# Kernel optimization log

Measured on AMD Instinct MI355X. Metric: run time of the kernel, lower is better.

## Reference

```python
import jax, jax.numpy as jnp
import numpy as np
import math

# Static config (mirrors init_kwargs)
E, B, S, D, F, HMAX = 8, 4, 1024, 1024, 4096, 8
W = 768                      # active slimmable width (multiple giving integer head_dim)
H = max(1, W * HMAX // D)    # = 6 heads at width 768
HD = W // H                  # = 128
TOPK = 2
EPS = 1e-6


def setup_inputs() -> dict:
    key = jax.random.key(0)
    ks = jax.random.split(key, 14)
    sd = 1.0 / math.sqrt(D)
    sf = 1.0 / math.sqrt(F)
    return {
        "x":  jax.random.normal(ks[0], (B, S, D), jnp.float32),
        "wr": jax.random.normal(ks[1], (D, E), jnp.float32) * sd,
        "qw": jax.random.normal(ks[2], (E, D, D), jnp.float32) * sd,
        "qb": jax.random.normal(ks[3], (E, D), jnp.float32) * sd,
        "kw": jax.random.normal(ks[4], (E, D, D), jnp.float32) * sd,
        "kb": jax.random.normal(ks[5], (E, D), jnp.float32) * sd,
        "vw": jax.random.normal(ks[6], (E, D, D), jnp.float32) * sd,
        "vb": jax.random.normal(ks[7], (E, D), jnp.float32) * sd,
        "ow": jax.random.normal(ks[8], (E, D, D), jnp.float32) * sd,
        "ob": jax.random.normal(ks[9], (E, D), jnp.float32) * sd,
        "w1": jax.random.normal(ks[10], (E, F, D), jnp.float32) * sd,
        "b1": jax.random.normal(ks[11], (E, F), jnp.float32) * sd,
        "w2": jax.random.normal(ks[12], (E, D, F), jnp.float32) * sf,
        "b2": jax.random.normal(ks[13], (E, D), jnp.float32) * sf,
    }


def _slim_linear(x, w, b, in_w, out_w):
    # SlimmableLinear: dynamically slice max-size weight/bias to active widths
    return x @ w[:out_w, :in_w].T + b[:out_w]


def _rms_norm(x):
    # SlimmableExpert._layer_norm: RMS normalization (no mean-subtract, no affine)
    var = jnp.mean(jnp.square(x), axis=-1, keepdims=True)
    return x / jnp.sqrt(var + EPS)


def _expert_fwd(x_s, qw, qb, kw, kb, vw, vb, ow, ob, w1, b1, w2, b2):
    # x_s: [B, S, W]  (already sliced to active width)
    # --- slimmable self-attention at width W ---
    q = _slim_linear(x_s, qw, qb, W, W).reshape(B, S, H, HD).transpose(0, 2, 1, 3)
    k = _slim_linear(x_s, kw, kb, W, W).reshape(B, S, H, HD).transpose(0, 2, 1, 3)
    v = _slim_linear(x_s, vw, vb, W, W).reshape(B, S, H, HD).transpose(0, 2, 1, 3)
    scores = jnp.einsum('bhqd,bhkd->bhqk', q, k) / math.sqrt(HD)   # [B,H,S,S]
    attn = jax.nn.softmax(scores, axis=-1)
    ao = jnp.einsum('bhqk,bhkd->bhqd', attn, v)
    ao = ao.transpose(0, 2, 1, 3).reshape(B, S, W)
    ao = _slim_linear(ao, ow, ob, W, W)
    x1 = _rms_norm(x_s + ao)
    # --- slimmable FFN: W -> F (full) -> W, exact GELU (torch default) ---
    h = jax.nn.gelu(_slim_linear(x1, w1, b1, W, F), approximate=False)
    f = _slim_linear(h, w2, b2, F, W)
    return _rms_norm(x1 + f)   # [B,S,W]


def reference(x, wr, qw, qb, kw, kb, vw, vb, ow, ob, w1, b1, w2, b2):
    # Router: softmax over experts, top-k dispatch with renormalized gates
    logits = jnp.einsum('bsd,de->bse', x, wr)            # [B,S,E]
    probs = jax.nn.softmax(logits, axis=-1)
    topv, topi = jax.lax.top_k(probs, TOPK)              # [B,S,K]
    topv = topv / jnp.sum(topv, axis=-1, keepdims=True)
    bi = jnp.arange(B)[:, None, None]
    si = jnp.arange(S)[None, :, None]
    gate = jnp.zeros((B, S, E), x.dtype).at[bi, si, topi].set(topv)  # sparse gate

    # Slice tokens to active width (width embedding skipped: closest stored
    # width 736 != 768, per source shape-match check)
    x_s = x[..., :W]
    outs = []
    for e in range(E):   # small fixed expert count; bounds peak memory
        outs.append(_expert_fwd(x_s, qw[e], qb[e], kw[e], kb[e], vw[e], vb[e],
                                ow[e], ob[e], w1[e], b1[e], w2[e], b2[e]))
    eo = jnp.stack(outs, axis=0)                          # [E,B,S,W]
    out_w = jnp.einsum('bse,ebsw->bsw', gate, eo)         # gate-weighted combine
    # Zero-pad sliced width back to full model dim (per SlimmableExpert)
    out = jnp.concatenate(
        [out_w, jnp.zeros((B, S, D - W), x.dtype)], axis=-1)
    return out
```

## Files before the change

kernel.cpp:

```cpp
#include <hip/hip_runtime.h>
#include <cstdint>

#define NE 8
#define NB 4
#define NS 1024
#define ND 1024
#define NF 4096
#define NW 768
#define NH 6
#define NHD 128
#define NTOK 4096
#define NBH 24
#define RCAP 10496
#define VSTRIDE ((size_t)NTOK * NW)
#define EPS 1e-6f

typedef unsigned short ush;
typedef __attribute__((ext_vector_type(8))) short short8;
typedef __attribute__((ext_vector_type(4))) float f32x4;
typedef __attribute__((ext_vector_type(4))) unsigned short u16x4;

typedef const __attribute__((address_space(1))) void gvoid_t;
typedef __attribute__((address_space(3))) void lvoid_t;

__device__ __forceinline__ void gload16(const void* g, void* l) {
  __builtin_amdgcn_global_load_lds((gvoid_t*)g, (lvoid_t*)l, 16, 0, 0);
}

__device__ __forceinline__ ush f2b(float f) {
  union { float f; uint32_t u; } x; x.f = f;
  uint32_t r = x.u + 0x7fffu + ((x.u >> 16) & 1u);
  return (ush)(r >> 16);
}
__device__ __forceinline__ float b2f(ush u) {
  union { uint32_t u; float f; } x; x.u = (uint32_t)u << 16;
  return x.f;
}
__device__ __forceinline__ int prefix_sum(const int* __restrict__ c, int n) {
  int s = 0;
#pragma unroll 1
  for (int i = 0; i < n; ++i) s += c[i];
  return s;
}


__global__ __launch_bounds__(256, 4)
void router_kernel(const float* __restrict__ x, const float* __restrict__ wr,
                   float* __restrict__ gate, int* __restrict__ inv) {
  int lane = threadIdx.x & 63, wave = threadIdx.x >> 6;
  int t = blockIdx.x * 4 + wave;
  float acc[NE] = {};
  for (int i = 0; i < 16; ++i) {
    int d = lane + i * 64;
    float xv = x[(size_t)t * ND + d];
    const float* wp = wr + (size_t)d * NE;
    float4 w0 = *(const float4*)wp, w1 = *(const float4*)(wp + 4);
    acc[0] += xv * w0.x; acc[1] += xv * w0.y; acc[2] += xv * w0.z; acc[3] += xv * w0.w;
    acc[4] += xv * w1.x; acc[5] += xv * w1.y; acc[6] += xv * w1.z; acc[7] += xv * w1.w;
  }
#pragma unroll
  for (int e = 0; e < NE; ++e)
    for (int m = 1; m < 64; m <<= 1) acc[e] += __shfl_xor(acc[e], m);
  int i1 = 0; float v1 = acc[0];
#pragma unroll
  for (int e = 1; e < NE; ++e) if (acc[e] > v1) { v1 = acc[e]; i1 = e; }
  int i2 = -1; float v2 = -3.0e38f;
#pragma unroll
  for (int e = 0; e < NE; ++e) if (e != i1 && acc[e] > v2) { v2 = acc[e]; i2 = e; }
  float p2 = __expf(v2 - v1);
  float g1 = 1.0f / (1.0f + p2), g2 = p2 / (1.0f + p2);
  if (lane < NE)
    gate[(size_t)t * NE + lane] = (lane == i1) ? g1 : ((lane == i2) ? g2 : 0.0f);
  if (lane < 2) inv[t * 2 + lane] = -1;
}

__global__ __launch_bounds__(1024, 1)
void build_index(const float* __restrict__ gate, int* __restrict__ cnt64s,
                 int* __restrict__ idx_all, int* __restrict__ inv) {
  int e = blockIdx.x >> 2, b = blockIdx.x & 3;
  int s = threadIdx.x, t = b * 1024 + s;
  bool on = gate[(size_t)t * NE + e] > 0.0f;
  idx_all[(e * 4 + b) * 1024 + s] = (b * 1024) | (int)0x80000000;
  __shared__ int wsum[16], wbase[16];
  unsigned long long mask = __ballot(on);
  int lane = s & 63, wv = s >> 6;
  if (lane == 0) wsum[wv] = __popcll(mask);
  __syncthreads();
  if (s == 0) {
    int acc = 0;
    for (int i = 0; i < 16; ++i) { wbase[i] = acc; acc += wsum[i]; }
    cnt64s[e * 4 + b] = (acc + 63) & ~63;
  }
  __syncthreads();
  if (on) {
    int pos = wbase[wv] + __popcll(mask & ((1ull << lane) - 1ull));
    idx_all[(e * 4 + b) * 1024 + pos] = t;
    int k = 0;
#pragma unroll
    for (int j = 0; j < NE; ++j) k += (j < e && gate[(size_t)t * NE + j] > 0.0f);
    inv[t * 2 + k] = (e << 12) | pos;
  }
}

__global__ __launch_bounds__(256, 4)
void cast_all(const float* __restrict__ x,
              const float* __restrict__ qw, const float* __restrict__ kw,
              const float* __restrict__ vw, const float* __restrict__ ow,
              const float* __restrict__ w1, const float* __restrict__ w2,
              ush* __restrict__ xs,
              ush* __restrict__ dq, ush* __restrict__ dk, ush* __restrict__ dv,
              ush* __restrict__ dwo, ush* __restrict__ d1, ush* __restrict__ d2) {
  int y = blockIdx.y;
  if (y == 8) {
    const int n4 = NTOK * NW / 4;
    for (int u = blockIdx.x * 256 + threadIdx.x; u < n4; u += gridDim.x * 256) {
      int r = u / (NW / 4), c = u - r * (NW / 4);
      float4 v = *(const float4*)(x + (size_t)r * ND + c * 4);
      u16x4 o; o.x = f2b(v.x); o.y = f2b(v.y); o.z = f2b(v.z); o.w = f2b(v.w);
      *(u16x4*)(xs + (size_t)u * 4) = o;
    }
    return;
  }
  const int e = y;
  const int Q4 = 147456;
  const int W14 = 786432;
  const int total = 4 * Q4 + 2 * W14;
  const float* qe = qw + (size_t)e * ND * ND;
  const float* ke = kw + (size_t)e * ND * ND;
  const float* ve = vw + (size_t)e * ND * ND;
  const float* oe = ow + (size_t)e * ND * ND;
  const float* w1e = w1 + (size_t)e * NF * ND;
  const float* w2e = w2 + (size_t)e * ND * NF;
  ush* dqe = dq + (size_t)e * NW * NW;
  ush* dke = dk + (size_t)e * NW * NW;
  ush* dve = dv + (size_t)e * NW * NW;
  ush* doe = dwo + (size_t)e * NW * NW;
  ush* d1e = d1 + (size_t)e * NF * NW;
  ush* d2e = d2 + (size_t)e * NW * NF;
  for (int u = blockIdx.x * 256 + threadIdx.x; u < total; u += gridDim.x * 256) {
    const float* src; ush* dst; int ldsrc, cols4, rel;
    if (u < 4 * Q4) {
      int which = u / Q4; rel = u - which * Q4;
      src = (which == 0) ? qe : (which == 1) ? ke : (which == 2) ? ve : oe;
      dst = (which == 0) ? dqe : (which == 1) ? dke : (which == 2) ? dve : doe;
      ldsrc = 1024; cols4 = 192;
    } else if (u < 4 * Q4 + W14) {
      rel = u - 4 * Q4; src = w1e; dst = d1e; ldsrc = 1024; cols4 = 192;
    } else {
      rel = u - 4 * Q4 - W14; src = w2e; dst = d2e; ldsrc = 4096; cols4 = 1024;
    }
    int r = rel / cols4, c = rel - r * cols4;
    float4 v = *(const float4*)(src + (size_t)r * ldsrc + (size_t)c * 4);
    u16x4 o; o.x = f2b(v.x); o.y = f2b(v.y); o.z = f2b(v.z); o.w = f2b(v.w);
    *(u16x4*)(dst + (size_t)rel * 4) = o;
  }
}

#define BM 128
#define BN 128

__device__ __forceinline__ float gelu_fast(float v) {
  float u = v * fmaf(0.0356774081f, v * v, 0.7978845608f);
  float p = __expf(2.0f * fabsf(u));
  float th = fmaf(-2.0f, __builtin_amdgcn_rcpf(p + 1.0f), 1.0f);
  th = copysignf(th, u);
  return 0.5f * v * (1.0f + th);
}

__device__ __forceinline__ void stage_geom(int tid, int c, int& row, int& kb) {
  int v = (c & 1) * 32 + (tid >> 3);
  int b67 = ((tid >> 2) & 1) ^ ((v >> 2) & 1);
  row = v + 64 * b67;
  kb = ((tid ^ v) & 3) << 4;
}

__global__ __launch_bounds__(256, 3)
void qkv_gemm(const ush* __restrict__ A,
              const ush* __restrict__ wqb, const ush* __restrict__ wkb,
              const ush* __restrict__ wvb,
              const float* __restrict__ qbias, const float* __restrict__ kbias,
              const float* __restrict__ vbias,
              ush* __restrict__ qg, ush* __restrict__ kg, ush* __restrict__ vtg,
              const int* __restrict__ cnt64s, const int* __restrict__ idx_all) {
  const int bid = blockIdx.x;
  const int e = bid & 7, wi = bid >> 3;
  const int bn = wi % 6, bm = (wi / 6) % 32, w = wi / 192;
  int sb = 0, cnt = 0;
  if (w == 0) {
    int sec = e * 4 + (bm >> 3);
    cnt = cnt64s[sec];
    if (((bm & 7) * 128) >= cnt) return;
    sb = prefix_sum(cnt64s, sec);
  }
  const ush* Bw = ((w == 0) ? wqb : (w == 1) ? wkb : wvb) + (size_t)e * NW * NW;
  const float* bias = ((w == 0) ? qbias : (w == 1) ? kbias : vbias) + (size_t)e * ND;

  __shared__ __align__(16) char LDS[3 * 16384];

  const int tid = threadIdx.x, lane = tid & 63, wave = tid >> 6;
  const int lr = lane & 15, lg = lane >> 4;
  const int wr = wave >> 1, wc = wave & 1;

  size_t srcOff[4];
#pragma unroll
  for (int c = 0; c < 4; ++c) {
    int row, kb; stage_geom(tid, c, row, kb);
    int gRow;
    if (c < 2) {
      if (w == 0) {
        int lrow = (bm & 7) * 128 + row;
        gRow = idx_all[(e * 4 + (bm >> 3)) * 1024 + lrow] & 0x7fffffff;
      } else {
        gRow = bm * BM + row;
      }
    } else {
      gRow = bn * BN + row;
    }
    srcOff[c] = (size_t)gRow * (NW * 2) + kb;
  }

  int offA[4], offB[4];
#pragma unroll
  for (int i = 0; i < 4; ++i) {
    offA[i] = (i * 16 + lr) * 128 + (((wr << 6) | (lg << 4)) ^ ((lr & 7) << 4));
    offB[i] = (i * 16 + lr) * 128 + (((wc << 6) | (lg << 4)) ^ ((lr & 7) << 4)) + 8192;
  }

  auto stg = [&](int slot, int kt) {
    size_t kOff = (size_t)kt * 64;
    char* dst = LDS + slot * 16384;
#pragma unroll
    for (int c = 0; c < 4; ++c) {
      const char* src = (c < 2) ? (const char*)A + srcOff[c] + kOff
                                : (const char*)Bw + srcOff[c] + kOff;
      gload16(src, dst + c * 4096 + tid * 16);
    }
  };

  f32x4 acc[4][4] = {};
  const int nkt = NW / 32;
  stg(0, 0); stg(1, 1);
  asm volatile("s_waitcnt vmcnt(4)" ::: "memory");
  asm volatile("s_barrier" ::: "memory");
  int slot = 0;
  for (int kt = 0; kt < nkt; ++kt) {
    int s2 = slot + 2; if (s2 >= 3) s2 -= 3;
    bool more = (kt + 2 < nkt);
    if (more) stg(s2, kt + 2);
    const char* base = LDS + slot * 16384;
    short8 af[4], bfr[4];
#pragma unroll
    for (int i = 0; i < 4; ++i) {
      af[i] = *(const short8*)(base + offA[i]);
      bfr[i] = *(const short8*)(base + offB[i]);
    }
#pragma unroll
    for (int i = 0; i < 4; ++i)
#pragma unroll
      for (int j = 0; j < 4; ++j)
        acc[i][j] = __builtin_amdgcn_mfma_f32_16x16x32_bf16(af[i], bfr[j], acc[i][j], 0, 0, 0);
    if (more) asm volatile("s_waitcnt vmcnt(4)" ::: "memory");
    else      asm volatile("s_waitcnt vmcnt(0)" ::: "memory");
    asm volatile("s_barrier" ::: "memory");
    slot = (slot == 2) ? 0 : slot + 1;
  }

#pragma unroll
  for (int i = 0; i < 4; ++i) {
    int lm16 = (bm & 7) * 128 + wr * 64 + i * 16;
    int m0 = bm * BM + wr * 64 + i * 16 + lg * 4;
#pragma unroll
    for (int j = 0; j < 4; ++j) {
      int n = bn * BN + wc * 64 + j * 16 + lr;
      float bb = bias[n];
      if (w == 0) {
        if (lm16 < cnt) {
          int grow = sb + lm16 + lg * 4;
#pragma unroll
          for (int r = 0; r < 4; ++r)
            qg[(size_t)(grow + r) * NW + n] = f2b(acc[i][j][r] + bb);
        }
      } else if (w == 1) {
        ush* o = kg + (size_t)e * NTOK * NW;
#pragma unroll
        for (int r = 0; r < 4; ++r)
          o[(size_t)(m0 + r) * NW + n] = f2b(acc[i][j][r] + bb);
      } else {
        int b_ = m0 >> 10, s0 = m0 & 1023, h_ = n >> 7, d = n & 127;
        u16x4 wv_;
#pragma unroll
        for (int r = 0; r < 4; ++r) wv_[r] = f2b(acc[i][j][r] + bb);
        *(u16x4*)(vtg + (size_t)e * VSTRIDE +
                  ((size_t)(b_ * NH + h_) * NHD + d) * NS + s0) = wv_;
      }
    }
  }
}

__global__ __launch_bounds__(256, 3)
void attn2(const ush* __restrict__ Qg, const ush* __restrict__ Kg,
           const ush* __restrict__ VTg,
           ush* __restrict__ po, float* __restrict__ mlm, float* __restrict__ mll,
           const int* __restrict__ cnt64s) {
  const int bid = blockIdx.x;
  const int e = bid & 7, wi = bid >> 3;
  const int qb = wi & 15, yy = wi >> 4;
  const int bh = yy >> 1, half = yy & 1;
  const int b = bh / NH, h = bh % NH;
  const int sec = e * 4 + b;
  const int cnt = cnt64s[sec];
  if (qb * 64 >= cnt) return;
  const int sb = prefix_sum(cnt64s, sec);

  __shared__ __align__(16) ush Ks[64 * 128];
  __shared__ __align__(16) ush VTs[128 * 64];
  __shared__ __align__(16) ush Ps[4 * 16 * 64];

  const int tid = threadIdx.x, lane = tid & 63, wave = tid >> 6;
  const int lr = lane & 15, lg = lane >> 4;
  const int k0 = half * 512;
  const float cexp = 1.4426950408889634f / sqrtf((float)NHD);

  const ush* Ke = Kg + (size_t)e * NTOK * NW;
  const ush* Ve = VTg + (size_t)e * VSTRIDE;

  int growq = sb + qb * 64 + wave * 16 + lr;
  short8 qf[4];
#pragma unroll
  for (int kk = 0; kk < 4; ++kk)
    qf[kk] = *(const short8*)(Qg + (size_t)growq * NW + h * NHD + kk * 32 + lg * 8);

  f32x4 accv[8] = {};
  float mr[4] = {-3.0e38f, -3.0e38f, -3.0e38f, -3.0e38f};
  float ls[4] = {};

  for (int kt = 0; kt < 8; ++kt) {
    __syncthreads();
#pragma unroll
    for (int p = 0; p < 4; ++p) {
      int o = p * 4096 + tid * 16;
      int row = o >> 8, cb = o & 255;
      gload16((const char*)Ke + ((size_t)(b * NS + k0 + kt * 64 + row) * NW + h * NHD) * 2 +
                  (cb ^ ((row & 7) << 4)),
              (char*)Ks + o);
    }
#pragma unroll
    for (int p = 0; p < 4; ++p) {
      int o = p * 4096 + tid * 16;
      int d = o >> 7, cb = o & 127;
      gload16((const char*)Ve + ((size_t)((b * NH + h) * NHD + d) * NS + k0 + kt * 64) * 2 +
                  (cb ^ ((d & 7) << 4)),
              (char*)VTs + o);
    }
    __syncthreads();

    f32x4 s[4] = {};
#pragma unroll
    for (int kg2 = 0; kg2 < 4; ++kg2)
#pragma unroll
      for (int kk = 0; kk < 4; ++kk) {
        int row = kg2 * 16 + lr;
        short8 kf = *(const short8*)((const char*)Ks + row * 256 +
                                     ((kk * 64 + lg * 16) ^ ((row & 7) << 4)));
        s[kg2] = __builtin_amdgcn_mfma_f32_16x16x32_bf16(qf[kk], kf, s[kg2], 0, 0, 0);
      }

    float mt[4];
#pragma unroll
    for (int r = 0; r < 4; ++r) {
      float m0 = fmaxf(fmaxf(s[0][r], s[1][r]), fmaxf(s[2][r], s[3][r]));
#pragma unroll
      for (int mm = 1; mm < 16; mm <<= 1) m0 = fmaxf(m0, __shfl_xor(m0, mm));
      mt[r] = m0;
    }
    bool need = (mt[0] > mr[0] + 8.f) || (mt[1] > mr[1] + 8.f) ||
                (mt[2] > mr[2] + 8.f) || (mt[3] > mr[3] + 8.f);
    if (__any(need)) {
#pragma unroll
      for (int r = 0; r < 4; ++r) {
        float mn = fmaxf(mr[r], mt[r]);
        float sc = exp2f((mr[r] - mn) * cexp);
        mr[r] = mn; ls[r] *= sc;
#pragma unroll
        for (int dg = 0; dg < 8; ++dg) accv[dg][r] *= sc;
      }
    }

    char* pw = (char*)Ps + wave * 2048;
#pragma unroll
    for (int kg2 = 0; kg2 < 4; ++kg2)
#pragma unroll
      for (int r = 0; r < 4; ++r) {
        float p = exp2f((s[kg2][r] - mr[r]) * cexp);
        ls[r] += p;
        int row = lg * 4 + r;
        *(ush*)(pw + row * 128 + (((kg2 * 16 + lr) * 2) ^ ((row & 7) << 4))) = f2b(p);
      }
    short8 pf[2];
#pragma unroll
    for (int kk2 = 0; kk2 < 2; ++kk2)
      pf[kk2] = *(const short8*)(pw + lr * 128 + ((kk2 * 64 + lg * 16) ^ ((lr & 7) << 4)));

#pragma unroll
    for (int dg = 0; dg < 8; ++dg) {
      int d = dg * 16 + lr;
#pragma unroll
      for (int kk2 = 0; kk2 < 2; ++kk2) {
        short8 vf = *(const short8*)((const char*)VTs + d * 128 +
                                     ((kk2 * 64 + lg * 16) ^ ((d & 7) << 4)));
        accv[dg] = __builtin_amdgcn_mfma_f32_16x16x32_bf16(pf[kk2], vf, accv[dg], 0, 0, 0);
      }
    }
  }

#pragma unroll
  for (int r = 0; r < 4; ++r)
#pragma unroll
    for (int mm = 1; mm < 16; mm <<= 1) ls[r] += __shfl_xor(ls[r], mm);

#pragma unroll
  for (int r = 0; r < 4; ++r) {
    int growr = sb + qb * 64 + wave * 16 + lg * 4 + r;
#pragma unroll
    for (int dg = 0; dg < 8; ++dg)
      po[((size_t)(growr * NH + h) * 2 + half) * NHD + dg * 16 + lr] = f2b(accv[dg][r]);
  }
  if (lr == 0) {
#pragma unroll
    for (int r = 0; r < 4; ++r) {
      int growr = sb + qb * 64 + wave * 16 + lg * 4 + r;
      mlm[(size_t)(growr * NH + h) * 2 + half] = mr[r];
      mll[(size_t)(growr * NH + h) * 2 + half] = ls[r];
    }
  }
}

__global__ __launch_bounds__(256, 4)
void attn_combine(const ush* __restrict__ po, const float* __restrict__ mlm,
                  const float* __restrict__ mll, ush* __restrict__ ao,
                  const int* __restrict__ cnt64s) {
  const float cexp = 1.4426950408889634f / sqrtf((float)NHD);
  int Rtot = prefix_sum(cnt64s, 32);
  int idx = blockIdx.x * 256 + threadIdx.x;
  int row = idx >> 4, dq = idx & 15;
  int grow = row / NH, h = row - grow * NH;
  if (grow >= Rtot) return;
  float m[2], l[2], M = -3.0e38f;
#pragma unroll
  for (int hh = 0; hh < 2; ++hh) {
    m[hh] = mlm[(size_t)row * 2 + hh];
    l[hh] = mll[(size_t)row * 2 + hh];
    M = fmaxf(M, m[hh]);
  }
  float L = 0.0f, w[2];
#pragma unroll
  for (int hh = 0; hh < 2; ++hh) { w[hh] = exp2f((m[hh] - M) * cexp); L += l[hh] * w[hh]; }
  float inv_ = 1.0f / L;
  float o[8] = {};
#pragma unroll
  for (int hh = 0; hh < 2; ++hh) {
    short8 v = *(const short8*)(po + ((size_t)row * 2 + hh) * NHD + dq * 8);
#pragma unroll
    for (int j = 0; j < 8; ++j) o[j] += b2f((ush)v[j]) * w[hh];
  }
  short8 res;
#pragma unroll
  for (int j = 0; j < 8; ++j) res[j] = (short)f2b(o[j] * inv_);
  *(short8*)(ao + (size_t)grow * NW + h * NHD + dq * 8) = res;
}

template <int EPI>
__global__ __launch_bounds__(256, 3)
void csr_gemm(const ush* __restrict__ A, const ush* __restrict__ Ball,
              const float* __restrict__ biasAll, ush* __restrict__ out,
              int N, int Kld, int klen, int nbn, int nbm, int nsplit,
              int strideBe, int biasStride,
              const int* __restrict__ cnt64s) {
  const int bid = blockIdx.x;
  const int e = bid & 7, wi = bid >> 3;
  const int bn = wi % nbn, bm = (wi / nbn) % nbm, s = wi / (nbn * nbm);
  const int Re = cnt64s[e * 4] + cnt64s[e * 4 + 1] + cnt64s[e * 4 + 2] + cnt64s[e * 4 + 3];
  if (bm * BM >= Re) return;
  const int ebase = prefix_sum(cnt64s, e * 4);
  const ush* Bw = Ball + (size_t)e * strideBe;
  const float* bias = (s == 0) ? biasAll + (size_t)e * biasStride : nullptr;
  const int koff = s * klen;
  ush* outp = out + (size_t)s * RCAP * N;

  __shared__ __align__(16) char LDS[3 * 16384];

  const int tid = threadIdx.x, lane = tid & 63, wave = tid >> 6;
  const int lr = lane & 15, lg = lane >> 4;
  const int wr = wave >> 1, wc = wave & 1;

  size_t srcOff[4];
#pragma unroll
  for (int c = 0; c < 4; ++c) {
    int row, kb; stage_geom(tid, c, row, kb);
    int gRow = (c < 2) ? (ebase + bm * BM + row) : (bn * BN + row);
    srcOff[c] = (size_t)gRow * (Kld * 2) + (size_t)koff * 2 + kb;
  }

  int offA[4], offB[4];
#pragma unroll
  for (int i = 0; i < 4; ++i) {
    offA[i] = (i * 16 + lr) * 128 + (((wr << 6) | (lg << 4)) ^ ((lr & 7) << 4));
    offB[i] = (i * 16 + lr) * 128 + (((wc << 6) | (lg << 4)) ^ ((lr & 7) << 4)) + 8192;
  }

  auto stg = [&](int slot, int kt) {
    size_t kOff = (size_t)kt * 64;
    char* dst = LDS + slot * 16384;
#pragma unroll
    for (int c = 0; c < 4; ++c) {
      const char* src = (c < 2) ? (const char*)A + srcOff[c] + kOff
                                : (const char*)Bw + srcOff[c] + kOff;
      gload16(src, dst + c * 4096 + tid * 16);
    }
  };

  f32x4 acc[4][4] = {};
  const int nkt = klen / 32;
  stg(0, 0); stg(1, 1);
  asm volatile("s_waitcnt vmcnt(4)" ::: "memory");
  asm volatile("s_barrier" ::: "memory");
  int slot = 0;
  for (int kt = 0; kt < nkt; ++kt) {
    int s2 = slot + 2; if (s2 >= 3) s2 -= 3;
    bool more = (kt + 2 < nkt);
    if (more) stg(s2, kt + 2);
    const char* base = LDS + slot * 16384;
    short8 af[4], bfr[4];
#pragma unroll
    for (int i = 0; i < 4; ++i) {
      af[i] = *(const short8*)(base + offA[i]);
      bfr[i] = *(const short8*)(base + offB[i]);
    }
#pragma unroll
    for (int i = 0; i < 4; ++i)
#pragma unroll
      for (int j = 0; j < 4; ++j)
        acc[i][j] = __builtin_amdgcn_mfma_f32_16x16x32_bf16(af[i], bfr[j], acc[i][j], 0, 0, 0);
    if (more) asm volatile("s_waitcnt vmcnt(4)" ::: "memory");
    else      asm volatile("s_waitcnt vmcnt(0)" ::: "memory");
    asm volatile("s_barrier" ::: "memory");
    slot = (slot == 2) ? 0 : slot + 1;
  }

#pragma unroll
  for (int i = 0; i < 4; ++i) {
    int lm16 = bm * BM + wr * 64 + i * 16;
    if (lm16 >= Re) continue;
#pragma unroll
    for (int j = 0; j < 4; ++j) {
      int n = bn * BN + wc * 64 + j * 16 + lr;
      float bb = bias ? bias[n] : 0.0f;
      int row0 = ebase + lm16 + lg * 4;
#pragma unroll
      for (int r = 0; r < 4; ++r) {
        float v = acc[i][j][r] + bb;
        if (EPI == 2) v = gelu_fast(v);
        outp[(size_t)(row0 + r) * N + n] = f2b(v);
      }
    }
  }
}

__global__ __launch_bounds__(256, 4)
void rmsnorm_res(const float* __restrict__ x, const ush* __restrict__ ooP,
                 ush* __restrict__ x1b, const int* __restrict__ cnt64s,
                 const int* __restrict__ idx_all) {
  int r = blockIdx.x;
  int base = 0, sec = -1, loc = 0;
#pragma unroll 1
  for (int i = 0; i < 32; ++i) {
    int cc = cnt64s[i];
    if (sec < 0 && r < base + cc) { sec = i; loc = r - base; }
    base += cc;
  }
  if (sec < 0) return;
  int t = idx_all[sec * 1024 + loc] & 0x7fffffff;
  __shared__ float red[4];
  int c = threadIdx.x, lane = c & 63, wave = c >> 6;
  float v[3]; float ss = 0.0f;
#pragma unroll
  for (int i = 0; i < 3; ++i) {
    int col = c + i * 256;
    float a = x[(size_t)t * ND + col] + b2f(ooP[(size_t)r * NW + col]) +
              b2f(ooP[(size_t)RCAP * NW + (size_t)r * NW + col]);
    v[i] = a; ss += a * a;
  }
#pragma unroll
  for (int m = 1; m < 64; m <<= 1) ss += __shfl_xor(ss, m);
  if (lane == 0) red[wave] = ss;
  __syncthreads();
  float tot = red[0] + red[1] + red[2] + red[3];
  float scale = rsqrtf(tot / (float)NW + EPS);
#pragma unroll
  for (int i = 0; i < 3; ++i) {
    int col = c + i * 256;
    x1b[(size_t)r * NW + col] = f2b(v[i] * scale);
  }
}

__global__ __launch_bounds__(256, 4)
void final_token(const ush* __restrict__ x1b, const ush* __restrict__ ffp,
                 const float* __restrict__ gate, const int* __restrict__ inv,
                 const int* __restrict__ cnt64s, float* __restrict__ out) {
  int t = blockIdx.x, c = threadIdx.x, lane = c & 63, wave = c >> 6;
  __shared__ float red[4];
  float acc[3] = {0.0f, 0.0f, 0.0f};
#pragma unroll 1
  for (int k = 0; k < 2; ++k) {
    int v = inv[t * 2 + k];
    if (v >= 0) {
      int e = v >> 12, pos = v & 0xfff;
      int b = t >> 10;
      int grow = prefix_sum(cnt64s, e * 4 + b) + pos;
      float g = gate[(size_t)t * NE + e];
      float vv[3]; float ss = 0.0f;
#pragma unroll
      for (int i = 0; i < 3; ++i) {
        int col = c + i * 256;
        float f = b2f(ffp[(size_t)grow * NW + col]) +
                  b2f(ffp[(size_t)RCAP * NW + (size_t)grow * NW + col]) +
                  b2f(ffp[2 * (size_t)RCAP * NW + (size_t)grow * NW + col]) +
                  b2f(ffp[3 * (size_t)RCAP * NW + (size_t)grow * NW + col]);
        float a = b2f(x1b[(size_t)grow * NW + col]) + f;
        vv[i] = a; ss += a * a;
      }
#pragma unroll
      for (int m = 1; m < 64; m <<= 1) ss += __shfl_xor(ss, m);
      if (lane == 0) red[wave] = ss;
      __syncthreads();
      float tot = red[0] + red[1] + red[2] + red[3];
      float scale = rsqrtf(tot / (float)NW + EPS) * g;
#pragma unroll
      for (int i = 0; i < 3; ++i) acc[i] += vv[i] * scale;
      __syncthreads();
    }
  }
#pragma unroll
  for (int i = 0; i < 3; ++i) out[(size_t)t * ND + c + i * 256] = acc[i];
  out[(size_t)t * ND + 768 + c] = 0.0f;
}

extern "C" void kernel_launch(void* const* d_in, const int* in_sizes, int n_in,
                              void* d_out, int out_size, void* d_ws, size_t ws_size,
                              hipStream_t stream) {
  (void)in_sizes; (void)n_in; (void)ws_size; (void)out_size;
  const float* x  = (const float*)d_in[0];
  const float* wr = (const float*)d_in[1];
  const float* qw = (const float*)d_in[2];
  const float* qbias = (const float*)d_in[3];
  const float* kw = (const float*)d_in[4];
  const float* kbias = (const float*)d_in[5];
  const float* vw = (const float*)d_in[6];
  const float* vbias = (const float*)d_in[7];
  const float* ow = (const float*)d_in[8];
  const float* obias = (const float*)d_in[9];
  const float* w1 = (const float*)d_in[10];
  const float* b1 = (const float*)d_in[11];
  const float* w2 = (const float*)d_in[12];
  const float* b2 = (const float*)d_in[13];
  float* out = (float*)d_out;
  char* ws = (char*)d_ws;

  size_t off = 0;
  auto alloc = [&](size_t bytes) {
    void* p = ws + off;
    off += (bytes + 255) & ~(size_t)255;
    return p;
  };
  float* gate = (float*)alloc((size_t)NTOK * NE * 4);
  int* cnt64s = (int*)alloc(32 * 4);
  int* idx_all = (int*)alloc((size_t)NE * NTOK * 4);
  int* inv = (int*)alloc((size_t)NTOK * 2 * 4);
  ush* xs  = (ush*)alloc((size_t)NTOK * NW * 2);
  ush* wqb = (ush*)alloc((size_t)NE * NW * NW * 2);
  ush* wkb = (ush*)alloc((size_t)NE * NW * NW * 2);
  ush* wvb = (ush*)alloc((size_t)NE * NW * NW * 2);
  ush* wob = (ush*)alloc((size_t)NE * NW * NW * 2);
  ush* w1b = (ush*)alloc((size_t)NE * NF * NW * 2);
  ush* w2b = (ush*)alloc((size_t)NE * NW * NF * 2);
  ush* x1b = (ush*)alloc((size_t)RCAP * NW * 2);
  char* arena1 = (char*)alloc((size_t)RCAP * NF * 2);
  ush* qg  = (ush*)arena1;
  ush* po  = (ush*)(arena1 + 16121856);
  float* mlm = (float*)(arena1 + 80609280);
  float* mll = (float*)(arena1 + 81616896);
  ush* hb  = (ush*)arena1;
  char* arena2 = (char*)alloc(112852992);
  ush* kg  = (ush*)arena2;
  ush* vtg = (ush*)(arena2 + 50331648);
  ush* aog = (ush*)arena2;
  ush* ooP = (ush*)(arena2 + 16121856);
  ush* ffp = (ush*)(arena2 + 48365568);

  router_kernel<<<dim3(NTOK / 4), 256, 0, stream>>>(x, wr, gate, inv);
  build_index<<<dim3(NE * NB), 1024, 0, stream>>>(gate, cnt64s, idx_all, inv);
  cast_all<<<dim3(288, 9), 256, 0, stream>>>(x, qw, kw, vw, ow, w1, w2,
                                             xs, wqb, wkb, wvb, wob, w1b, w2b);

  qkv_gemm<<<dim3(8 * 576), 256, 0, stream>>>(
      xs, wqb, wkb, wvb, qbias, kbias, vbias, qg, kg, vtg, cnt64s, idx_all);

  attn2<<<dim3(8 * 768), 256, 0, stream>>>(qg, kg, vtg, po, mlm, mll, cnt64s);
  attn_combine<<<dim3(RCAP * NH * 16 / 256), 256, 0, stream>>>(po, mlm, mll, aog, cnt64s);

  csr_gemm<0><<<dim3(8 * 384), 256, 0, stream>>>(
      aog, wob, obias, ooP, NW, NW, 384, 6, 32, 2, NW * NW, ND, cnt64s);

  rmsnorm_res<<<dim3(RCAP), 256, 0, stream>>>(x, ooP, x1b, cnt64s, idx_all);

  csr_gemm<2><<<dim3(8 * 1024), 256, 0, stream>>>(
      x1b, w1b, b1, hb, NF, NW, NW, 32, 32, 1, NF * NW, NF, cnt64s);

  csr_gemm<0><<<dim3(8 * 768), 256, 0, stream>>>(
      hb, w2b, b2, ffp, NW, NF, 1024, 6, 32, 4, NW * NF, ND, cnt64s);

  final_token<<<dim3(NTOK), 256, 0, stream>>>(x1b, ffp, gate, inv, cnt64s, out);
}
```

Measured before the change: 595.9 us.

## Widen QKV and FFN-up GEMM tiles to 128x256 and raise MFMA priority

The QKV projection and the FFN up-projection (with GELU) now use 128x256 output tiles. Each wave computes 4x8 MFMA fragments, so every A fragment loaded from LDS is reused across twice as many columns, and the grid has half as many blocks. A new csr_gemm_w kernel replaces csr_gemm<2> for the FFN up-projection, and the GELU epilogue is removed from the generic template. s_setprio is raised around the MFMA loops in all GEMMs and in attention so waves issuing matrix work get priority. The larger tiles use more LDS and accumulator registers, so occupancy drops to 2 blocks per CU.

New measurement: 586.0 us. About the same (-1.7%).

```diff
diff --git a/kernel.cpp b/kernel.cpp
--- a/kernel.cpp
+++ b/kernel.cpp
@@ -167,14 +167,12 @@
   return 0.5f * v * (1.0f + th);
 }
 
-__device__ __forceinline__ void stage_geom(int tid, int c, int& row, int& kb) {
-  int v = (c & 1) * 32 + (tid >> 3);
-  int b67 = ((tid >> 2) & 1) ^ ((v >> 2) & 1);
-  row = v + 64 * b67;
-  kb = ((tid ^ v) & 3) << 4;
-}
-
-__global__ __launch_bounds__(256, 3)
+__device__ __forceinline__ void stage_geom2(int tid, int u, int PAIR, int& row, int& kb) {
+  row = u + PAIR * (((tid >> 2) ^ (u >> 2)) & 1);
+  kb = ((tid ^ u) & 3) << 4;
+}
+
+__global__ __launch_bounds__(256, 2)
 void qkv_gemm(const ush* __restrict__ A,
               const ush* __restrict__ wqb, const ush* __restrict__ wkb,
               const ush* __restrict__ wvb,
@@ -184,7 +182,7 @@
               const int* __restrict__ cnt64s, const int* __restrict__ idx_all) {
   const int bid = blockIdx.x;
   const int e = bid & 7, wi = bid >> 3;
-  const int bn = wi % 6, bm = (wi / 6) % 32, w = wi / 192;
+  const int bn = wi % 3, bm = (wi / 3) % 32, w = wi / 96;
   int sb = 0, cnt = 0;
   if (w == 0) {
     int sec = e * 4 + (bm >> 3);
@@ -195,71 +193,76 @@
   const ush* Bw = ((w == 0) ? wqb : (w == 1) ? wkb : wvb) + (size_t)e * NW * NW;
   const float* bias = ((w == 0) ? qbias : (w == 1) ? kbias : vbias) + (size_t)e * ND;
 
-  __shared__ __align__(16) char LDS[3 * 16384];
+  __shared__ __align__(16) char LDS[3 * 24576];
 
   const int tid = threadIdx.x, lane = tid & 63, wave = tid >> 6;
   const int lr = lane & 15, lg = lane >> 4;
   const int wr = wave >> 1, wc = wave & 1;
 
-  size_t srcOff[4];
+  size_t srcOff[6];
+#pragma unroll
+  for (int c = 0; c < 2; ++c) {
+    int u = c * 32 + (tid >> 3), row, kb;
+    stage_geom2(tid, u, 64, row, kb);
+    int gRow;
+    if (w == 0) {
+      int lrow = (bm & 7) * 128 + row;
+      gRow = idx_all[(e * 4 + (bm >> 3)) * 1024 + lrow] & 0x7fffffff;
+    } else {
+      gRow = bm * BM + row;
+    }
+    srcOff[c] = (size_t)gRow * (NW * 2) + kb;
+  }
 #pragma unroll
   for (int c = 0; c < 4; ++c) {
-    int row, kb; stage_geom(tid, c, row, kb);
-    int gRow;
-    if (c < 2) {
-      if (w == 0) {
-        int lrow = (bm & 7) * 128 + row;
-        gRow = idx_all[(e * 4 + (bm >> 3)) * 1024 + lrow] & 0x7fffffff;
-      } else {
-        gRow = bm * BM + row;
-      }
-    } else {
-      gRow = bn * BN + row;
-    }
-    srcOff[c] = (size_t)gRow * (NW * 2) + kb;
-  }
-
-  int offA[4], offB[4];
-#pragma unroll
-  for (int i = 0; i < 4; ++i) {
+    int u = c * 32 + (tid >> 3), row, kb;
+    stage_geom2(tid, u, 128, row, kb);
+    srcOff[2 + c] = (size_t)(bn * 256 + row) * (NW * 2) + kb;
+  }
+
+  int offA[4], offB[8];
+#pragma unroll
+  for (int i = 0; i < 4; ++i)
     offA[i] = (i * 16 + lr) * 128 + (((wr << 6) | (lg << 4)) ^ ((lr & 7) << 4));
-    offB[i] = (i * 16 + lr) * 128 + (((wc << 6) | (lg << 4)) ^ ((lr & 7) << 4)) + 8192;
-  }
+#pragma unroll
+  for (int j = 0; j < 8; ++j)
+    offB[j] = (j * 16 + lr) * 128 + (((wc << 6) | (lg << 4)) ^ ((lr & 7) << 4)) + 8192;
 
   auto stg = [&](int slot, int kt) {
     size_t kOff = (size_t)kt * 64;
-    char* dst = LDS + slot * 16384;
-#pragma unroll
-    for (int c = 0; c < 4; ++c) {
-      const char* src = (c < 2) ? (const char*)A + srcOff[c] + kOff
-                                : (const char*)Bw + srcOff[c] + kOff;
-      gload16(src, dst + c * 4096 + tid * 16);
-    }
+    char* dst = LDS + slot * 24576;
+#pragma unroll
+    for (int c = 0; c < 2; ++c)
+      gload16((const char*)A + srcOff[c] + kOff, dst + c * 4096 + tid * 16);
+#pragma unroll
+    for (int c = 0; c < 4; ++c)
+      gload16((const char*)Bw + srcOff[2 + c] + kOff, dst + 8192 + c * 4096 + tid * 16);
   };
 
-  f32x4 acc[4][4] = {};
+  f32x4 acc[4][8] = {};
   const int nkt = NW / 32;
   stg(0, 0); stg(1, 1);
-  asm volatile("s_waitcnt vmcnt(4)" ::: "memory");
+  asm volatile("s_waitcnt vmcnt(6)" ::: "memory");
   asm volatile("s_barrier" ::: "memory");
   int slot = 0;
   for (int kt = 0; kt < nkt; ++kt) {
     int s2 = slot + 2; if (s2 >= 3) s2 -= 3;
     bool more = (kt + 2 < nkt);
     if (more) stg(s2, kt + 2);
-    const char* base = LDS + slot * 16384;
-    short8 af[4], bfr[4];
-#pragma unroll
-    for (int i = 0; i < 4; ++i) {
-      af[i] = *(const short8*)(base + offA[i]);
-      bfr[i] = *(const short8*)(base + offB[i]);
-    }
+    const char* base = LDS + slot * 24576;
+    short8 af[4], bfr[8];
+#pragma unroll
+    for (int i = 0; i < 4; ++i) af[i] = *(const short8*)(base + offA[i]);
+#pragma unroll
+    for (int j = 0; j < 8; ++j) bfr[j] = *(const short8*)(base + offB[j]);
+    __builtin_amdgcn_s_setprio(1);
 #pragma unroll
     for (int i = 0; i < 4; ++i)
 #pragma unroll
-      for (int j = 0; j < 4; ++j)
+      for (int j = 0; j < 8; ++j)
         acc[i][j] = __builtin_amdgcn_mfma_f32_16x16x32_bf16(af[i], bfr[j], acc[i][j], 0, 0, 0);
-    if (more) asm volatile("s_waitcnt vmcnt(4)" ::: "memory");
+    __builtin_amdgcn_s_setprio(0);
+    if (more) asm volatile("s_waitcnt vmcnt(6)" ::: "memory");
     else      asm volatile("s_waitcnt vmcnt(0)" ::: "memory");
     asm volatile("s_barrier" ::: "memory");
     slot = (slot == 2) ? 0 : slot + 1;
@@ -270,8 +273,8 @@
     int lm16 = (bm & 7) * 128 + wr * 64 + i * 16;
     int m0 = bm * BM + wr * 64 + i * 16 + lg * 4;
 #pragma unroll
-    for (int j = 0; j < 4; ++j) {
-      int n = bn * BN + wc * 64 + j * 16 + lr;
+    for (int j = 0; j < 8; ++j) {
+      int n = bn * 256 + wc * 128 + j * 16 + lr;
       float bb = bias[n];
       if (w == 0) {
         if (lm16 < cnt) {
@@ -355,6 +358,7 @@
     __syncthreads();
 
     f32x4 s[4] = {};
+    __builtin_amdgcn_s_setprio(1);
 #pragma unroll
     for (int kg2 = 0; kg2 < 4; ++kg2)
 #pragma unroll
@@ -364,6 +368,7 @@
                                      ((kk * 64 + lg * 16) ^ ((row & 7) << 4)));
         s[kg2] = __builtin_amdgcn_mfma_f32_16x16x32_bf16(qf[kk], kf, s[kg2], 0, 0, 0);
       }
+    __builtin_amdgcn_s_setprio(0);
 
     float mt[4];
 #pragma unroll
@@ -401,6 +406,7 @@
     for (int kk2 = 0; kk2 < 2; ++kk2)
       pf[kk2] = *(const short8*)(pw + lr * 128 + ((kk2 * 64 + lg * 16) ^ ((lr & 7) << 4)));
 
+    __builtin_amdgcn_s_setprio(1);
 #pragma unroll
     for (int dg = 0; dg < 8; ++dg) {
       int d = dg * 16 + lr;
@@ -411,6 +417,7 @@
         accv[dg] = __builtin_amdgcn_mfma_f32_16x16x32_bf16(pf[kk2], vf, accv[dg], 0, 0, 0);
       }
     }
+    __builtin_amdgcn_s_setprio(0);
   }
 
 #pragma unroll
@@ -467,6 +474,105 @@
 #pragma unroll
   for (int j = 0; j < 8; ++j) res[j] = (short)f2b(o[j] * inv_);
   *(short8*)(ao + (size_t)grow * NW + h * NHD + dq * 8) = res;
+}
+
+__global__ __launch_bounds__(256, 2)
+void csr_gemm_w(const ush* __restrict__ A, const ush* __restrict__ Ball,
+                const float* __restrict__ biasAll, ush* __restrict__ out,
+                int N, int Kld, int klen, int nbn,
+                int strideBe, int biasStride,
+                const int* __restrict__ cnt64s) {
+  const int bid = blockIdx.x;
+  const int e = bid & 7, wi = bid >> 3;
+  const int bn = wi % nbn, bm = wi / nbn;
+  const int Re = cnt64s[e * 4] + cnt64s[e * 4 + 1] + cnt64s[e * 4 + 2] + cnt64s[e * 4 + 3];
+  if (bm * BM >= Re) return;
+  const int ebase = prefix_sum(cnt64s, e * 4);
+  const ush* Bw = Ball + (size_t)e * strideBe;
+  const float* bias = biasAll + (size_t)e * biasStride;
+
+  __shared__ __align__(16) char LDS[3 * 24576];
+
+  const int tid = threadIdx.x, lane = tid & 63, wave = tid >> 6;
+  const int lr = lane & 15, lg = lane >> 4;
+  const int wr = wave >> 1, wc = wave & 1;
+
+  size_t srcOff[6];
+#pragma unroll
+  for (int c = 0; c < 2; ++c) {
+    int u = c * 32 + (tid >> 3), row, kb;
+    stage_geom2(tid, u, 64, row, kb);
+    srcOff[c] = (size_t)(ebase + bm * BM + row) * (Kld * 2) + kb;
+  }
+#pragma unroll
+  for (int c = 0; c < 4; ++c) {
+    int u = c * 32 + (tid >> 3), row, kb;
+    stage_geom2(tid, u, 128, row, kb);
+    srcOff[2 + c] = (size_t)(bn * 256 + row) * (Kld * 2) + kb;
+  }
+
+  int offA[4], offB[8];
+#pragma unroll
+  for (int i = 0; i < 4; ++i)
+    offA[i] = (i * 16 + lr) * 128 + (((wr << 6) | (lg << 4)) ^ ((lr & 7) << 4));
+#pragma unroll
+  for (int j = 0; j < 8; ++j)
+    offB[j] = (j * 16 + lr) * 128 + (((wc << 6) | (lg << 4)) ^ ((lr & 7) << 4)) + 8192;
+
+  auto stg = [&](int slot, int kt) {
+    size_t kOff = (size_t)kt * 64;
+    char* dst = LDS + slot * 24576;
+#pragma unroll
+    for (int c = 0; c < 2; ++c)
+      gload16((const char*)A + srcOff[c] + kOff, dst + c * 4096 + tid * 16);
+#pragma unroll
+    for (int c = 0; c < 4; ++c)
+      gload16((const char*)Bw + srcOff[2 + c] + kOff, dst + 8192 + c * 4096 + tid * 16);
+  };
+
+  f32x4 acc[4][8] = {};
+  const int nkt = klen / 32;
+  stg(0, 0); stg(1, 1);
+  asm volatile("s_waitcnt vmcnt(6)" ::: "memory");
+  asm volatile("s_barrier" ::: "memory");
+  int slot = 0;
+  for (int kt = 0; kt < nkt; ++kt) {
+    int s2 = slot + 2; if (s2 >= 3) s2 -= 3;
+    bool more = (kt + 2 < nkt);
+    if (more) stg(s2, kt + 2);
+    const char* base = LDS + slot * 24576;
+    short8 af[4], bfr[8];
+#pragma unroll
+    for (int i = 0; i < 4; ++i) af[i] = *(const short8*)(base + offA[i]);
+#pragma unroll
+    for (int j = 0; j < 8; ++j) bfr[j] = *(const short8*)(base + offB[j]);
+    __builtin_amdgcn_s_setprio(1);
+#pragma unroll
+    for (int i = 0; i < 4; ++i)
+#pragma unroll
+      for (int j = 0; j < 8; ++j)
+        acc[i][j] = __builtin_amdgcn_mfma_f32_16x16x32_bf16(af[i], bfr[j], acc[i][j], 0, 0, 0);
+    __builtin_amdgcn_s_setprio(0);
+    if (more) asm volatile("s_waitcnt vmcnt(6)" ::: "memory");
+    else      asm volatile("s_waitcnt vmcnt(0)" ::: "memory");
+    asm volatile("s_barrier" ::: "memory");
+    slot = (slot == 2) ? 0 : slot + 1;
+  }
+
+#pragma unroll
+  for (int i = 0; i < 4; ++i) {
+    int lm16 = bm * BM + wr * 64 + i * 16;
+    if (lm16 >= Re) continue;
+#pragma unroll
+    for (int j = 0; j < 8; ++j) {
+      int n = bn * 256 + wc * 128 + j * 16 + lr;
+      float bb = bias[n];
+      int row0 = ebase + lm16 + lg * 4;
+#pragma unroll
+      for (int r = 0; r < 4; ++r)
+        out[(size_t)(row0 + r) * N + n] = f2b(gelu_fast(acc[i][j][r] + bb));
+    }
+  }
 }
 
 template <int EPI>
@@ -496,7 +602,8 @@
   size_t srcOff[4];
 #pragma unroll
   for (int c = 0; c < 4; ++c) {
-    int row, kb; stage_geom(tid, c, row, kb);
+    int u = (c & 1) * 32 + (tid >> 3), row, kb;
+    stage_geom2(tid, u, 64, row, kb);
     int gRow = (c < 2) ? (ebase + bm * BM + row) : (bn * BN + row);
     srcOff[c] = (size_t)gRow * (Kld * 2) + (size_t)koff * 2 + kb;
   }
@@ -536,11 +643,13 @@
       af[i] = *(const short8*)(base + offA[i]);
       bfr[i] = *(const short8*)(base + offB[i]);
     }
+    __builtin_amdgcn_s_setprio(1);
 #pragma unroll
     for (int i = 0; i < 4; ++i)
 #pragma unroll
       for (int j = 0; j < 4; ++j)
         acc[i][j] = __builtin_amdgcn_mfma_f32_16x16x32_bf16(af[i], bfr[j], acc[i][j], 0, 0, 0);
+    __builtin_amdgcn_s_setprio(0);
     if (more) asm volatile("s_waitcnt vmcnt(4)" ::: "memory");
     else      asm volatile("s_waitcnt vmcnt(0)" ::: "memory");
     asm volatile("s_barrier" ::: "memory");
@@ -557,11 +666,8 @@
       float bb = bias ? bias[n] : 0.0f;
       int row0 = ebase + lm16 + lg * 4;
 #pragma unroll
-      for (int r = 0; r < 4; ++r) {
-        float v = acc[i][j][r] + bb;
-        if (EPI == 2) v = gelu_fast(v);
-        outp[(size_t)(row0 + r) * N + n] = f2b(v);
-      }
+      for (int r = 0; r < 4; ++r)
+        outp[(size_t)(row0 + r) * N + n] = f2b(acc[i][j][r] + bb);
     }
   }
 }
@@ -702,7 +808,7 @@
   cast_all<<<dim3(288, 9), 256, 0, stream>>>(x, qw, kw, vw, ow, w1, w2,
                                              xs, wqb, wkb, wvb, wob, w1b, w2b);
 
-  qkv_gemm<<<dim3(8 * 576), 256, 0, stream>>>(
+  qkv_gemm<<<dim3(8 * 288), 256, 0, stream>>>(
       xs, wqb, wkb, wvb, qbias, kbias, vbias, qg, kg, vtg, cnt64s, idx_all);
 
   attn2<<<dim3(8 * 768), 256, 0, stream>>>(qg, kg, vtg, po, mlm, mll, cnt64s);
@@ -713,8 +819,8 @@
 
   rmsnorm_res<<<dim3(RCAP), 256, 0, stream>>>(x, ooP, x1b, cnt64s, idx_all);
 
-  csr_gemm<2><<<dim3(8 * 1024), 256, 0, stream>>>(
-      x1b, w1b, b1, hb, NF, NW, NW, 32, 32, 1, NF * NW, NF, cnt64s);
+  csr_gemm_w<<<dim3(8 * 512), 256, 0, stream>>>(
+      x1b, w1b, b1, hb, NF, NW, NW, 16, NF * NW, NF, cnt64s);
 
   csr_gemm<0><<<dim3(8 * 768), 256, 0, stream>>>(
       hb, w2b, b2, ffp, NW, NF, 1024, 6, 32, 4, NW * NF, ND, cnt64s);
```
